# Performance work log

Measured on AMD Instinct MI355X. Metric: run time of the kernel, lower is better.

## Reference

```python
import jax, jax.numpy as jnp
import numpy as np

PATCH = 9
EMBED = 768

def setup_inputs() -> dict:
    key = jax.random.key(0)
    k1, k2, k3, k4, k5, k6 = jax.random.split(key, 6)
    B, T, C, H, W = 4, 16, 3, 256, 256
    N = 8192
    patch_dim = PATCH * PATCH * C  # 243
    frames = jax.random.normal(k1, (B, T, C, H, W), dtype=jnp.float32)
    coords = jax.random.uniform(k2, (B, N, 2), dtype=jnp.float32)
    t_src = jax.random.randint(k3, (B, N), 0, T, dtype=jnp.int32)
    # MLP params (Linear: y = x @ W + b), kaiming-ish scale
    W1 = jax.random.normal(k4, (patch_dim, EMBED), dtype=jnp.float32) / np.sqrt(patch_dim)
    b1 = jnp.zeros((EMBED,), dtype=jnp.float32)
    W2 = jax.random.normal(k5, (EMBED, EMBED), dtype=jnp.float32) / np.sqrt(EMBED)
    b2 = jnp.zeros((EMBED,), dtype=jnp.float32)
    return {"frames": frames, "coords": coords, "t_src": t_src,
            "W1": W1, "b1": b1, "W2": W2, "b2": b2}

def reference(frames, coords, t_src, W1, b1, W2, b2):
    B, T, C, H, W = frames.shape
    N = coords.shape[1]
    half = PATCH // 2
    # integer center pixel (coords in [0,1] -> truncation == floor for nonneg)
    u = (coords[..., 0] * (W - 1)).astype(jnp.int32)  # (B, N)
    v = (coords[..., 1] * (H - 1)).astype(jnp.int32)
    off = jnp.arange(PATCH, dtype=jnp.int32) - half    # (P,)
    # replicate padding at borders == clamped gather indices
    ys = jnp.clip(v[..., None] + off, 0, H - 1)        # (B, N, P)
    xs = jnp.clip(u[..., None] + off, 0, W - 1)        # (B, N, P)
    fp = jnp.transpose(frames, (0, 1, 3, 4, 2))        # (B, T, H, W, C)
    bidx = jnp.arange(B, dtype=jnp.int32)[:, None, None, None]
    # gather patches: (B, N, P, P, C)
    patches = fp[bidx, t_src[:, :, None, None].astype(jnp.int32),
                 ys[:, :, :, None], xs[:, :, None, :]]
    x = patches.reshape(B, N, PATCH * PATCH * C)       # (B, N, 243)
    h = jax.nn.gelu(x @ W1 + b1, approximate=False)    # torch nn.GELU = exact erf
    return h @ W2 + b2                                 # (B, N, EMBED)
```

## Files before the change

kernel.cpp:

```cpp
#include <hip/hip_runtime.h>
#include <math.h>


typedef __attribute__((ext_vector_type(8))) short short8;
typedef __attribute__((ext_vector_type(4))) float floatx4;

#define M_ROWS 32768
#define KPAD   256
#define EMB    768

__device__ __forceinline__ unsigned short f2bf(float f) {
    union { float f; unsigned int i; } w;
    w.f = f;
    unsigned int x = w.i;
    x += 0x7fffu + ((x >> 16) & 1u);
    return (unsigned short)(x >> 16);
}

__global__ void k_transpose_w1(const float* __restrict__ W1,
                               unsigned short* __restrict__ W1T) {
    int idx = blockIdx.x * 256 + threadIdx.x;
    int n = idx >> 8;
    int k = idx & 255;
    W1T[idx] = (k < 243) ? f2bf(W1[k * EMB + n]) : (unsigned short)0;
}

__global__ void k_transpose_w2(const float* __restrict__ W2,
                               unsigned short* __restrict__ W2T) {
    int idx = blockIdx.x * 256 + threadIdx.x;
    int n = idx / EMB;
    int k = idx - n * EMB;
    W2T[idx] = f2bf(W2[k * EMB + n]);
}

__global__ void k_gather(const float* __restrict__ frames,
                         const float* __restrict__ coords,
                         const int* __restrict__ t_src,
                         unsigned short* __restrict__ X) {
    int row  = blockIdx.x * 4 + (threadIdx.x >> 6);
    int lane = threadIdx.x & 63;
    int b = row >> 13;

    float cu = coords[row * 2 + 0];
    float cv = coords[row * 2 + 1];
    int u = (int)(cu * 255.0f);
    int v = (int)(cv * 255.0f);
    int t = t_src[row];

    const float* fb = frames + (size_t)(b * 16 + t) * (3 * 256 * 256);
    unsigned short* xr = X + (size_t)row * KPAD;

#pragma unroll
    for (int it = 0; it < 4; ++it) {
        int e = lane + it * 64;
        unsigned short val = 0;
        if (e < 243) {
            int c  = e % 3;
            int ij = e / 3;
            int j  = ij % 9;
            int i  = ij / 9;
            int y = v + i - 4; y = (y < 0) ? 0 : (y > 255 ? 255 : y);
            int x = u + j - 4; x = (x < 0) ? 0 : (x > 255 ? 255 : x);
            val = f2bf(fb[(size_t)c * 65536 + y * 256 + x]);
        }
        xr[e] = val;
    }
}

template <int K, bool GELU, bool OUT_F32>
__global__ __launch_bounds__(256)
void k_gemm(const unsigned short* __restrict__ A,
            const unsigned short* __restrict__ BT,
            const float* __restrict__ bias,
            void* __restrict__ Cv) {
    const int BK = 64, LDK = 72;
    __shared__ unsigned short As[128 * LDK];
    __shared__ unsigned short Bs[128 * LDK];

    int tid  = threadIdx.x;
    int wave = tid >> 6;
    int lane = tid & 63;
    int wm = (wave >> 1) * 64;
    int wn = (wave & 1) * 64;
    int lm = lane & 15;
    int lq = lane >> 4;

    int m0 = blockIdx.x * 128;
    int n0 = blockIdx.y * 128;

    floatx4 acc[4][4];
#pragma unroll
    for (int i = 0; i < 4; ++i)
#pragma unroll
        for (int j = 0; j < 4; ++j)
            acc[i][j] = (floatx4){0.f, 0.f, 0.f, 0.f};

    const unsigned short* Ag = A  + (size_t)m0 * K;
    const unsigned short* Bg = BT + (size_t)n0 * K;

    for (int k0 = 0; k0 < K; k0 += BK) {
#pragma unroll
        for (int i = 0; i < 4; ++i) {
            int chunk = tid + i * 256;
            int r  = chunk >> 3;
            int kc = (chunk & 7) << 3;
            short8 va = *(const short8*)(Ag + (size_t)r * K + k0 + kc);
            *(short8*)(&As[r * LDK + kc]) = va;
            short8 vb = *(const short8*)(Bg + (size_t)r * K + k0 + kc);
            *(short8*)(&Bs[r * LDK + kc]) = vb;
        }
        __syncthreads();

#pragma unroll
        for (int ks = 0; ks < 2; ++ks) {
            short8 af[4], bf[4];
#pragma unroll
            for (int mi = 0; mi < 4; ++mi)
                af[mi] = *(const short8*)(&As[(wm + mi * 16 + lm) * LDK + ks * 32 + lq * 8]);
#pragma unroll
            for (int ni = 0; ni < 4; ++ni)
                bf[ni] = *(const short8*)(&Bs[(wn + ni * 16 + lm) * LDK + ks * 32 + lq * 8]);
#pragma unroll
            for (int mi = 0; mi < 4; ++mi)
#pragma unroll
                for (int ni = 0; ni < 4; ++ni)
                    acc[mi][ni] = __builtin_amdgcn_mfma_f32_16x16x32_bf16(
                        af[mi], bf[ni], acc[mi][ni], 0, 0, 0);
        }
        __syncthreads();
    }

#pragma unroll
    for (int ni = 0; ni < 4; ++ni) {
        int col = n0 + wn + ni * 16 + lm;
        float bs = bias[col];
#pragma unroll
        for (int mi = 0; mi < 4; ++mi) {
            int rowb = m0 + wm + mi * 16 + lq * 4;
#pragma unroll
            for (int r = 0; r < 4; ++r) {
                float x = acc[mi][ni][r] + bs;
                if (GELU)
                    x = 0.5f * x * (1.0f + erff(x * 0.70710678118f));
                size_t idx = (size_t)(rowb + r) * EMB + col;
                if (OUT_F32)
                    ((float*)Cv)[idx] = x;
                else
                    ((unsigned short*)Cv)[idx] = f2bf(x);
            }
        }
    }
}

extern "C" void kernel_launch(void* const* d_in, const int* in_sizes, int n_in,
                              void* d_out, int out_size, void* d_ws, size_t ws_size,
                              hipStream_t stream) {
    const float* frames = (const float*)d_in[0];
    const float* coords = (const float*)d_in[1];
    const int*   t_src  = (const int*)d_in[2];
    const float* W1     = (const float*)d_in[3];
    const float* b1     = (const float*)d_in[4];
    const float* W2     = (const float*)d_in[5];
    const float* b2     = (const float*)d_in[6];
    float* out = (float*)d_out;

    char* ws = (char*)d_ws;
    unsigned short* X    = (unsigned short*)(ws);
    unsigned short* Hbuf = (unsigned short*)(ws + 16777216);
    unsigned short* W1T  = (unsigned short*)(ws + 16777216 + 50331648);
    unsigned short* W2T  = (unsigned short*)(ws + 16777216 + 50331648 + 393216);

    k_transpose_w1<<<768, 256, 0, stream>>>(W1, W1T);
    k_transpose_w2<<<2304, 256, 0, stream>>>(W2, W2T);

    k_gather<<<M_ROWS / 4, 256, 0, stream>>>(frames, coords, t_src, X);

    k_gemm<KPAD, true, false><<<dim3(M_ROWS / 128, EMB / 128), 256, 0, stream>>>(X, W1T, b1, Hbuf);

    k_gemm<EMB, false, true><<<dim3(M_ROWS / 128, EMB / 128), 256, 0, stream>>>(Hbuf, W2T, b2, out);
}
```

Baseline: 269.3 us.

## Load GEMM tiles directly to LDS with XOR swizzle, reorder patch K layout

The GEMM now uses global_load_lds to copy A/B tiles straight into shared memory instead of staging them through registers, with an XOR swizzle in place of padding to avoid bank conflicts. Launch bounds now request 3 blocks per CU. The patch feature order is permuted to channel-major, with W1 rows permuted to match, so gather lanes read more contiguous pixels. W2's transpose goes through a shared-memory tile so reads and writes are coalesced. The risk is correctness of the swizzle and LDS-load addressing, plus register pressure from the occupancy hint.

```diff
diff --git a/kernel.cpp b/kernel.cpp
--- a/kernel.cpp
+++ b/kernel.cpp
@@ -8,6 +8,9 @@
 #define M_ROWS 32768
 #define KPAD   256
 #define EMB    768
+
+typedef __attribute__((address_space(1))) const void g_void;
+typedef __attribute__((address_space(3))) void l_void;
 
 __device__ __forceinline__ unsigned short f2bf(float f) {
     union { float f; unsigned int i; } w;
@@ -20,17 +23,32 @@
 __global__ void k_transpose_w1(const float* __restrict__ W1,
                                unsigned short* __restrict__ W1T) {
     int idx = blockIdx.x * 256 + threadIdx.x;
-    int n = idx >> 8;
-    int k = idx & 255;
-    W1T[idx] = (k < 243) ? f2bf(W1[k * EMB + n]) : (unsigned short)0;
+    int n  = idx >> 8;
+    int kp = idx & 255;
+    unsigned short v = 0;
+    if (kp < 243) {
+        int c = kp / 81;
+        int r = kp - c * 81;
+        int i = r / 9;
+        int j = r - i * 9;
+        int e = i * 27 + j * 3 + c;
+        v = f2bf(W1[e * EMB + n]);
+    }
+    W1T[idx] = v;
 }
 
 __global__ void k_transpose_w2(const float* __restrict__ W2,
                                unsigned short* __restrict__ W2T) {
-    int idx = blockIdx.x * 256 + threadIdx.x;
-    int n = idx / EMB;
-    int k = idx - n * EMB;
-    W2T[idx] = f2bf(W2[k * EMB + n]);
+    __shared__ float tile[32][33];
+    int tx = threadIdx.x & 31, ty = threadIdx.x >> 5;
+    int k0 = blockIdx.x * 32, n0 = blockIdx.y * 32;
+#pragma unroll
+    for (int i = 0; i < 4; ++i)
+        tile[ty + i * 8][tx] = W2[(size_t)(k0 + ty + i * 8) * EMB + n0 + tx];
+    __syncthreads();
+#pragma unroll
+    for (int i = 0; i < 4; ++i)
+        W2T[(size_t)(n0 + ty + i * 8) * EMB + k0 + tx] = f2bf(tile[tx][ty + i * 8]);
 }
 
 __global__ void k_gather(const float* __restrict__ frames,
@@ -52,30 +70,29 @@
 
 #pragma unroll
     for (int it = 0; it < 4; ++it) {
-        int e = lane + it * 64;
+        int kp = lane + it * 64;
         unsigned short val = 0;
-        if (e < 243) {
-            int c  = e % 3;
-            int ij = e / 3;
-            int j  = ij % 9;
-            int i  = ij / 9;
+        if (kp < 243) {
+            int c = kp / 81;
+            int r = kp - c * 81;
+            int i = r / 9;
+            int j = r - i * 9;
             int y = v + i - 4; y = (y < 0) ? 0 : (y > 255 ? 255 : y);
             int x = u + j - 4; x = (x < 0) ? 0 : (x > 255 ? 255 : x);
             val = f2bf(fb[(size_t)c * 65536 + y * 256 + x]);
         }
-        xr[e] = val;
+        xr[kp] = val;
     }
 }
 
 template <int K, bool GELU, bool OUT_F32>
-__global__ __launch_bounds__(256)
+__global__ __launch_bounds__(256, 3)
 void k_gemm(const unsigned short* __restrict__ A,
             const unsigned short* __restrict__ BT,
             const float* __restrict__ bias,
             void* __restrict__ Cv) {
-    const int BK = 64, LDK = 72;
-    __shared__ unsigned short As[128 * LDK];
-    __shared__ unsigned short Bs[128 * LDK];
+    __shared__ unsigned short As[128 * 64];
+    __shared__ unsigned short Bs[128 * 64];
 
     int tid  = threadIdx.x;
     int wave = tid >> 6;
@@ -98,34 +115,43 @@
     const unsigned short* Ag = A  + (size_t)m0 * K;
     const unsigned short* Bg = BT + (size_t)n0 * K;
 
-    for (int k0 = 0; k0 < K; k0 += BK) {
+    int rl    = lane >> 3;
+    int pslot = lane & 7;
+
+    for (int k0 = 0; k0 < K; k0 += 64) {
 #pragma unroll
         for (int i = 0; i < 4; ++i) {
-            int chunk = tid + i * 256;
-            int r  = chunk >> 3;
-            int kc = (chunk & 7) << 3;
-            short8 va = *(const short8*)(Ag + (size_t)r * K + k0 + kc);
-            *(short8*)(&As[r * LDK + kc]) = va;
-            short8 vb = *(const short8*)(Bg + (size_t)r * K + k0 + kc);
-            *(short8*)(&Bs[r * LDK + kc]) = vb;
+            int chunk = wave * 4 + i;
+            int r     = chunk * 8 + rl;
+            int lslot = pslot ^ (r & 7);
+            const unsigned short* ga = Ag + (size_t)r * K + k0 + (lslot << 3);
+            const unsigned short* gb = Bg + (size_t)r * K + k0 + (lslot << 3);
+            __builtin_amdgcn_global_load_lds((g_void*)ga, (l_void*)(As + chunk * 512), 16, 0, 0);
+            __builtin_amdgcn_global_load_lds((g_void*)gb, (l_void*)(Bs + chunk * 512), 16, 0, 0);
         }
         __syncthreads();
 
 #pragma unroll
         for (int ks = 0; ks < 2; ++ks) {
-            short8 af[4], bf[4];
-#pragma unroll
-            for (int mi = 0; mi < 4; ++mi)
-                af[mi] = *(const short8*)(&As[(wm + mi * 16 + lm) * LDK + ks * 32 + lq * 8]);
-#pragma unroll
-            for (int ni = 0; ni < 4; ++ni)
-                bf[ni] = *(const short8*)(&Bs[(wn + ni * 16 + lm) * LDK + ks * 32 + lq * 8]);
+            short8 af[4], bfr[4];
+#pragma unroll
+            for (int mi = 0; mi < 4; ++mi) {
+                int row = wm + mi * 16 + lm;
+                int ps  = ((ks << 2) + lq) ^ (row & 7);
+                af[mi] = *(const short8*)(As + row * 64 + (ps << 3));
+            }
+#pragma unroll
+            for (int ni = 0; ni < 4; ++ni) {
+                int row = wn + ni * 16 + lm;
+                int ps  = ((ks << 2) + lq) ^ (row & 7);
+                bfr[ni] = *(const short8*)(Bs + row * 64 + (ps << 3));
+            }
 #pragma unroll
             for (int mi = 0; mi < 4; ++mi)
 #pragma unroll
                 for (int ni = 0; ni < 4; ++ni)
                     acc[mi][ni] = __builtin_amdgcn_mfma_f32_16x16x32_bf16(
-                        af[mi], bf[ni], acc[mi][ni], 0, 0, 0);
+                        af[mi], bfr[ni], acc[mi][ni], 0, 0, 0);
         }
         __syncthreads();
     }
@@ -171,7 +197,7 @@
     unsigned short* W2T  = (unsigned short*)(ws + 16777216 + 50331648 + 393216);
 
     k_transpose_w1<<<768, 256, 0, stream>>>(W1, W1T);
-    k_transpose_w2<<<2304, 256, 0, stream>>>(W2, W2T);
+    k_transpose_w2<<<dim3(24, 24), 256, 0, stream>>>(W2, W2T);
 
     k_gather<<<M_ROWS / 4, 256, 0, stream>>>(frames, coords, t_src, X);
 
```

Result: faster. 244.5 us (-9.2%).
